# Optimization experiments

Hardware: AMD Instinct MI355X
Metric: run time of the kernel (lower is better)

Reference implementation:

```python
import jax, jax.numpy as jnp
import numpy as np

B, L, C, R = 4, 2048, 64, 8
A_SCALE = 0.1  # keeps spectral radius of per-step A < 1 so 2048-step products stay stable


def setup_inputs() -> dict:
    key = jax.random.key(0)
    k1, k2, k3, k4 = jax.random.split(key, 4)
    A_re = jax.random.normal(k1, (B, L, C, R, R), jnp.float32) * A_SCALE
    A_im = jax.random.normal(k2, (B, L, C, R, R), jnp.float32) * A_SCALE
    X_re = jax.random.normal(k3, (B, L, C, R), jnp.float32)
    X_im = jax.random.normal(k4, (B, L, C, R), jnp.float32)
    return {"A_re": A_re, "A_im": A_im, "X_re": X_re, "X_im": X_im}


def reference(A_re, A_im, X_re, X_im):
    # Complex linear recurrence: Y_t = A_t @ Y_{t-1} + X_t (Y_0 = X_0),
    # computed as a parallel associative scan over the L axis, matching
    # the Triton combine_fn: (a1,x1) o (a2,x2) = (a2@a1, a2@x1 + x2).
    A = jax.lax.complex(A_re, A_im)  # [B,L,C,R,R] complex64
    X = jax.lax.complex(X_re, X_im)  # [B,L,C,R]   complex64

    def combine(left, right):
        a1, x1 = left
        a2, x2 = right
        new_a = jnp.matmul(a2, a1)                          # [.,R,R]@[.,R,R]
        new_x = jnp.einsum('...ij,...j->...i', a2, x1) + x2  # [.,R,R]@[.,R]
        return (new_a, new_x)

    _, Y = jax.lax.associative_scan(combine, (A, X), axis=1)
    # Return real/imag stacked so the output dtype is float32: [B,L,C,R,2]
    return jnp.stack((jnp.real(Y), jnp.imag(Y)), axis=-1)
```

## Files before the change

### kernel.cpp

```cpp
#include <hip/hip_runtime.h>

#define B 4
#define L 2048
#define C 64
#define R 8
#define NCH (B * C)
#define TQ 16
#define S (L / TQ)
#define GRP (NCH / 8)


__global__ __launch_bounds__(64) void k_summary(
    const float* __restrict__ Are, const float* __restrict__ Aim,
    const float* __restrict__ Xre, const float* __restrict__ Xim,
    float2* __restrict__ sumP, float2* __restrict__ sumQ)
{
    __shared__ __align__(16) float sm[1152];
    const int lane = threadIdx.x;
    const int c = lane >> 3, r = lane & 7;
    const int s = blockIdx.x >> 5;
    const int g = blockIdx.x & 31;
    const int n0 = g * 8;
    const int b = n0 >> 6;
    const int cc0 = n0 & (C - 1);
    const int n = n0 + c;
    const int tbase = s * TQ;
    const int sIdx = c * 16 + ((r ^ c) << 1);

    float Pre[8], Pim[8];
#pragma unroll
    for (int k = 0; k < 8; ++k) { Pre[k] = (k == r) ? 1.f : 0.f; Pim[k] = 0.f; }
    float qre = 0.f, qim = 0.f;

    float4 sa0, sa1, si0, si1; float sxr, sxi;
    float4 ta0, ta1, ti0, ti1; float txr, txi;

#define LOADSET1(t, A0, A1, I0, I1, XR, XI)                                    \
    {                                                                          \
        const int fb = (b * L + (t)) * C + cc0;                                \
        const float4* pA = (const float4*)(Are + (long)fb * 64) + lane * 2;    \
        const float4* pI = (const float4*)(Aim + (long)fb * 64) + lane * 2;    \
        A0 = pA[0]; A1 = pA[1]; I0 = pI[0]; I1 = pI[1];                        \
        XR = Xre[(long)fb * 8 + lane]; XI = Xim[(long)fb * 8 + lane];          \
    }

#define STAGESET1(A0, A1, I0, I1, XR, XI)                                      \
    {                                                                          \
        float4* s4 = (float4*)sm;                                              \
        s4[sIdx] = A0; s4[sIdx + 1] = A1;                                      \
        s4[128 + sIdx] = I0; s4[128 + sIdx + 1] = I1;                          \
        sm[1024 + lane] = XR; sm[1088 + lane] = XI;                            \
    }

#define COMPUTE_STEP1()                                                        \
    {                                                                          \
        float xr[8], xi[8];                                                    \
        *(float4*)&xr[0] = *(const float4*)(sm + 1024 + c * 8);                \
        *(float4*)&xr[4] = *(const float4*)(sm + 1024 + c * 8 + 4);            \
        *(float4*)&xi[0] = *(const float4*)(sm + 1088 + c * 8);                \
        *(float4*)&xi[4] = *(const float4*)(sm + 1088 + c * 8 + 4);            \
        _Pragma("unroll")                                                      \
        for (int k = 0; k < 8; ++k) {                                          \
            qre += Pre[k] * xr[k] - Pim[k] * xi[k];                            \
            qim += Pre[k] * xi[k] + Pim[k] * xr[k];                            \
        }                                                                      \
        float Nre[8], Nim[8];                                                  \
        _Pragma("unroll")                                                      \
        for (int j = 0; j < 8; ++j) { Nre[j] = 0.f; Nim[j] = 0.f; }            \
        _Pragma("unroll")                                                      \
        for (int k = 0; k < 8; ++k) {                                          \
            const int ko = ((k ^ c) << 3);    \
            float er[8], ei[8];                                                \
            *(float4*)&er[0] = *(const float4*)(sm + c * 64 + ko);             \
            *(float4*)&er[4] = *(const float4*)(sm + c * 64 + ko + 4);         \
            *(float4*)&ei[0] = *(const float4*)(sm + 512 + c * 64 + ko);       \
            *(float4*)&ei[4] = *(const float4*)(sm + 512 + c * 64 + ko + 4);   \
            const float pr = Pre[k], pi = Pim[k];                              \
            _Pragma("unroll")                                                  \
            for (int j = 0; j < 8; ++j) {                                      \
                Nre[j] += pr * er[j] - pi * ei[j];                             \
                Nim[j] += pr * ei[j] + pi * er[j];                             \
            }                                                                  \
        }                                                                      \
        _Pragma("unroll")                                                      \
        for (int k = 0; k < 8; ++k) { Pre[k] = Nre[k]; Pim[k] = Nim[k]; }      \
    }

    LOADSET1(tbase + TQ - 1, sa0, sa1, si0, si1, sxr, sxi);
    LOADSET1(tbase + TQ - 2, ta0, ta1, ti0, ti1, txr, txi);

#pragma unroll 1
    for (int tt = TQ - 1; tt >= 1; tt -= 2) {
        STAGESET1(sa0, sa1, si0, si1, sxr, sxi);
        if (tt >= 3) LOADSET1(tbase + tt - 2, sa0, sa1, si0, si1, sxr, sxi);
        COMPUTE_STEP1();
        STAGESET1(ta0, ta1, ti0, ti1, txr, txi);
        if (tt >= 3) LOADSET1(tbase + tt - 3, ta0, ta1, ti0, ti1, txr, txi);
        COMPUTE_STEP1();
    }

    float4* gp = (float4*)(sumP + ((long)(s * 256 + n) * 8 + r) * 8);
    gp[0] = make_float4(Pre[0], Pim[0], Pre[1], Pim[1]);
    gp[1] = make_float4(Pre[2], Pim[2], Pre[3], Pim[3]);
    gp[2] = make_float4(Pre[4], Pim[4], Pre[5], Pim[5]);
    gp[3] = make_float4(Pre[6], Pim[6], Pre[7], Pim[7]);
    sumQ[(long)(s * 256 + n) * 8 + r] = make_float2(qre, qim);
}

__global__ __launch_bounds__(64) void k_carry(
    const float2* __restrict__ sumP, const float2* __restrict__ sumQ,
    float2* __restrict__ carry)
{
    __shared__ __align__(16) float cb[160];
    const int lane = threadIdx.x;
    const int c = lane >> 3, r = lane & 7;
    const int n = blockIdx.x * 8 + c;

    float yr = 0.f, yi = 0.f;
    long base = (long)n * 8;
    const float4* prow0 = (const float4*)(sumP + (base + r) * 8);
    float4 p0 = prow0[0], p1 = prow0[1], p2 = prow0[2], p3 = prow0[3];
    float2 qv = sumQ[base + r];

#pragma unroll 1
    for (int s = 0; s < S; ++s) {
        carry[base + r] = make_float2(yr, yi);
        *(float2*)(cb + c * 20 + 2 * r) = make_float2(yr, yi);
        float4 w0 = p0, w1 = p1, w2 = p2, w3 = p3;
        float2 q = qv;
        if (s + 1 < S) {
            const long nb = base + 2048;
            const float4* np = (const float4*)(sumP + (nb + r) * 8);
            p0 = np[0]; p1 = np[1]; p2 = np[2]; p3 = np[3];
            qv = sumQ[nb + r];
        }
        float yvr[8], yvi[8];
        {
            float4 u0 = *(const float4*)(cb + c * 20);
            float4 u1 = *(const float4*)(cb + c * 20 + 4);
            float4 u2 = *(const float4*)(cb + c * 20 + 8);
            float4 u3 = *(const float4*)(cb + c * 20 + 12);
            yvr[0]=u0.x; yvi[0]=u0.y; yvr[1]=u0.z; yvi[1]=u0.w;
            yvr[2]=u1.x; yvi[2]=u1.y; yvr[3]=u1.z; yvi[3]=u1.w;
            yvr[4]=u2.x; yvi[4]=u2.y; yvr[5]=u2.z; yvi[5]=u2.w;
            yvr[6]=u3.x; yvi[6]=u3.y; yvr[7]=u3.z; yvi[7]=u3.w;
        }
        float prr[8], pri[8];
        prr[0]=w0.x; pri[0]=w0.y; prr[1]=w0.z; pri[1]=w0.w;
        prr[2]=w1.x; pri[2]=w1.y; prr[3]=w1.z; pri[3]=w1.w;
        prr[4]=w2.x; pri[4]=w2.y; prr[5]=w2.z; pri[5]=w2.w;
        prr[6]=w3.x; pri[6]=w3.y; prr[7]=w3.z; pri[7]=w3.w;
        float nr0 = q.x, ni0 = q.y, nr1 = 0.f, ni1 = 0.f;
#pragma unroll
        for (int k = 0; k < 8; k += 2) {
            nr0 += prr[k] * yvr[k] - pri[k] * yvi[k];
            ni0 += prr[k] * yvi[k] + pri[k] * yvr[k];
            nr1 += prr[k+1] * yvr[k+1] - pri[k+1] * yvi[k+1];
            ni1 += prr[k+1] * yvi[k+1] + pri[k+1] * yvr[k+1];
        }
        yr = nr0 + nr1; yi = ni0 + ni1;
        base += 2048;
    }
}

__global__ __launch_bounds__(64) void k_fixup(
    const float* __restrict__ Are, const float* __restrict__ Aim,
    const float* __restrict__ Xre, const float* __restrict__ Xim,
    const float2* __restrict__ carry, float2* __restrict__ out)
{
    __shared__ __align__(16) float cb[160];
    const int lane = threadIdx.x;
    const int c = lane >> 3, r = lane & 7;
    const int blk = (int)gridDim.x - 1 - (int)blockIdx.x;
    const int s = blk >> 5;
    const int g = blk & 31;
    const int n0 = g * 8;
    const int b = n0 >> 6;
    const int cc0 = n0 & (C - 1);
    const int n = n0 + c;
    const int tbase = s * TQ;

    float yvr[8], yvi[8];
    {
        const float4* cv = (const float4*)(carry + (long)(s * 256 + n) * 8);
        float4 w0 = cv[0], w1 = cv[1], w2 = cv[2], w3 = cv[3];
        yvr[0]=w0.x; yvi[0]=w0.y; yvr[1]=w0.z; yvi[1]=w0.w;
        yvr[2]=w1.x; yvi[2]=w1.y; yvr[3]=w1.z; yvi[3]=w1.w;
        yvr[4]=w2.x; yvi[4]=w2.y; yvr[5]=w2.z; yvi[5]=w2.w;
        yvr[6]=w3.x; yvi[6]=w3.y; yvr[7]=w3.z; yvi[7]=w3.w;
    }

    float4 sa0, sa1, si0, si1; float sxr, sxi;
    float4 ta0, ta1, ti0, ti1; float txr, txi;

#define LOADSET3(t, A0, A1, I0, I1, XR, XI)                                    \
    {                                                                          \
        const int fb = (b * L + (t)) * C + cc0;                                \
        const float4* pA = (const float4*)(Are + (long)fb * 64) + lane * 2;    \
        const float4* pI = (const float4*)(Aim + (long)fb * 64) + lane * 2;    \
        A0 = pA[0]; A1 = pA[1]; I0 = pI[0]; I1 = pI[1];                        \
        XR = Xre[(long)fb * 8 + lane]; XI = Xim[(long)fb * 8 + lane];          \
    }

#define FIX_STEP(A0, A1, I0, I1, XR_, XI_, t)                                  \
    {                                                                          \
        float nr0 = (XR_), ni0 = (XI_), nr1 = 0.f, ni1 = 0.f;                  \
        nr0 += A0.x * yvr[0] - I0.x * yvi[0];                                  \
        ni0 += A0.x * yvi[0] + I0.x * yvr[0];                                  \
        nr1 += A0.y * yvr[1] - I0.y * yvi[1];                                  \
        ni1 += A0.y * yvi[1] + I0.y * yvr[1];                                  \
        nr0 += A0.z * yvr[2] - I0.z * yvi[2];                                  \
        ni0 += A0.z * yvi[2] + I0.z * yvr[2];                                  \
        nr1 += A0.w * yvr[3] - I0.w * yvi[3];                                  \
        ni1 += A0.w * yvi[3] + I0.w * yvr[3];                                  \
        nr0 += A1.x * yvr[4] - I1.x * yvi[4];                                  \
        ni0 += A1.x * yvi[4] + I1.x * yvr[4];                                  \
        nr1 += A1.y * yvr[5] - I1.y * yvi[5];                                  \
        ni1 += A1.y * yvi[5] + I1.y * yvr[5];                                  \
        nr0 += A1.z * yvr[6] - I1.z * yvi[6];                                  \
        ni0 += A1.z * yvi[6] + I1.z * yvr[6];                                  \
        nr1 += A1.w * yvr[7] - I1.w * yvi[7];                                  \
        ni1 += A1.w * yvi[7] + I1.w * yvr[7];                                  \
        const float nr = nr0 + nr1, ni = ni0 + ni1;                            \
        const int fb = (b * L + (t)) * C + cc0;                                \
        out[(long)fb * 8 + lane] = make_float2(nr, ni);                        \
        *(float2*)(cb + c * 20 + 2 * r) = make_float2(nr, ni);                 \
        float4 u0 = *(const float4*)(cb + c * 20);                             \
        float4 u1 = *(const float4*)(cb + c * 20 + 4);                         \
        float4 u2 = *(const float4*)(cb + c * 20 + 8);                         \
        float4 u3 = *(const float4*)(cb + c * 20 + 12);                        \
        yvr[0]=u0.x; yvi[0]=u0.y; yvr[1]=u0.z; yvi[1]=u0.w;                    \
        yvr[2]=u1.x; yvi[2]=u1.y; yvr[3]=u1.z; yvi[3]=u1.w;                    \
        yvr[4]=u2.x; yvi[4]=u2.y; yvr[5]=u2.z; yvi[5]=u2.w;                    \
        yvr[6]=u3.x; yvi[6]=u3.y; yvr[7]=u3.z; yvi[7]=u3.w;                    \
    }

    LOADSET3(tbase + 0, sa0, sa1, si0, si1, sxr, sxi);
    LOADSET3(tbase + 1, ta0, ta1, ti0, ti1, txr, txi);

#pragma unroll 1
    for (int tt = 0; tt < TQ; tt += 2) {
        float4 A0 = sa0, A1 = sa1, I0 = si0, I1 = si1;
        float XR = sxr, XI = sxi;
        if (tt + 2 < TQ) LOADSET3(tbase + tt + 2, sa0, sa1, si0, si1, sxr, sxi);
        FIX_STEP(A0, A1, I0, I1, XR, XI, tbase + tt);
        float4 B0 = ta0, B1 = ta1, J0 = ti0, J1 = ti1;
        float YR = txr, YI = txi;
        if (tt + 3 < TQ) LOADSET3(tbase + tt + 3, ta0, ta1, ti0, ti1, txr, txi);
        FIX_STEP(B0, B1, J0, J1, YR, YI, tbase + tt + 1);
    }
}

extern "C" void kernel_launch(void* const* d_in, const int* in_sizes, int n_in,
                              void* d_out, int out_size, void* d_ws, size_t ws_size,
                              hipStream_t stream)
{
    const float* Are = (const float*)d_in[0];
    const float* Aim = (const float*)d_in[1];
    const float* Xre = (const float*)d_in[2];
    const float* Xim = (const float*)d_in[3];
    float2* out = (float2*)d_out;

    float2* sumP  = (float2*)d_ws;
    float2* sumQ  = sumP + (long)S * NCH * 64;
    float2* carry = sumQ + (long)S * NCH * 8;

    k_summary<<<S * GRP, 64, 0, stream>>>(Are, Aim, Xre, Xim, sumP, sumQ);
    k_carry<<<NCH / 8, 64, 0, stream>>>(sumP, sumQ, carry);
    k_fixup<<<S * GRP, 64, 0, stream>>>(Are, Aim, Xre, Xim, carry, out);
}
```

Measured before the change: 432.5 us.

## Use async global-to-LDS loads, 4-wave blocks, and shuffles for vector broadcast

The summary kernel now streams A and X tiles straight into double-buffered LDS with global_load_lds and explicit vmcnt waits, replacing the register staging and LDS store round trip. Both the summary and fixup kernels pack four independent wavefronts per 256-thread block. The carry and fixup kernels broadcast the state vector with cross-lane shuffles instead of an LDS write/read. This is meant to cut load latency and LDS traffic, but it relies on hand-written waitcnt accounting and needs more LDS per block.

```diff
diff --git a/kernel.cpp b/kernel.cpp
--- a/kernel.cpp
+++ b/kernel.cpp
@@ -10,55 +10,62 @@
 #define GRP (NCH / 8)
 
 
-__global__ __launch_bounds__(64) void k_summary(
+#define GLL(gp, lp, sz)                                                        \
+    __builtin_amdgcn_global_load_lds(                                          \
+        (const __attribute__((address_space(1))) void*)(gp),                   \
+        (__attribute__((address_space(3))) void*)(lp), sz, 0, 0)
+
+__global__ __launch_bounds__(256) void k_summary(
     const float* __restrict__ Are, const float* __restrict__ Aim,
     const float* __restrict__ Xre, const float* __restrict__ Xim,
     float2* __restrict__ sumP, float2* __restrict__ sumQ)
 {
-    __shared__ __align__(16) float sm[1152];
-    const int lane = threadIdx.x;
+    __shared__ __align__(16) float sm[4 * 2 * 1152];
+    const int lane = threadIdx.x & 63;
+    const int w = __builtin_amdgcn_readfirstlane((int)(threadIdx.x >> 6));
     const int c = lane >> 3, r = lane & 7;
-    const int s = blockIdx.x >> 5;
-    const int g = blockIdx.x & 31;
+    const int s = blockIdx.x >> 3;
+    const int g = (blockIdx.x & 7) * 4 + w;
     const int n0 = g * 8;
     const int b = n0 >> 6;
     const int cc0 = n0 & (C - 1);
     const int n = n0 + c;
     const int tbase = s * TQ;
-    const int sIdx = c * 16 + ((r ^ c) << 1);
+
+    const int q = (lane >> 1) & 7, h = lane & 1;
+    const int c0 = lane >> 4, c1 = 4 + (lane >> 4);
+    const int o0 = c0 * 16 + ((q ^ c0) << 1) + h;
+    const int o1 = c1 * 16 + ((q ^ c1) << 1) + h;
+
+    char* lw = ((char*)sm) + w * 9216;
+    const float* wb = sm + w * 2304;
 
     float Pre[8], Pim[8];
 #pragma unroll
     for (int k = 0; k < 8; ++k) { Pre[k] = (k == r) ? 1.f : 0.f; Pim[k] = 0.f; }
     float qre = 0.f, qim = 0.f;
 
-    float4 sa0, sa1, si0, si1; float sxr, sxi;
-    float4 ta0, ta1, ti0, ti1; float txr, txi;
-
-#define LOADSET1(t, A0, A1, I0, I1, XR, XI)                                    \
+#define ISSUE1(t, bf)                                                          \
     {                                                                          \
         const int fb = (b * L + (t)) * C + cc0;                                \
-        const float4* pA = (const float4*)(Are + (long)fb * 64) + lane * 2;    \
-        const float4* pI = (const float4*)(Aim + (long)fb * 64) + lane * 2;    \
-        A0 = pA[0]; A1 = pA[1]; I0 = pI[0]; I1 = pI[1];                        \
-        XR = Xre[(long)fb * 8 + lane]; XI = Xim[(long)fb * 8 + lane];          \
-    }
-
-#define STAGESET1(A0, A1, I0, I1, XR, XI)                                      \
-    {                                                                          \
-        float4* s4 = (float4*)sm;                                              \
-        s4[sIdx] = A0; s4[sIdx + 1] = A1;                                      \
-        s4[128 + sIdx] = I0; s4[128 + sIdx + 1] = I1;                          \
-        sm[1024 + lane] = XR; sm[1088 + lane] = XI;                            \
-    }
-
-#define COMPUTE_STEP1()                                                        \
+        const float4* gA = (const float4*)(Are + (long)fb * 64);               \
+        const float4* gI = (const float4*)(Aim + (long)fb * 64);               \
+        char* lb = lw + (bf) * 4608;                                           \
+        GLL(gA + o0, lb, 16);                                                  \
+        GLL(gA + o1, lb + 1024, 16);                                           \
+        GLL(gI + o0, lb + 2048, 16);                                           \
+        GLL(gI + o1, lb + 3072, 16);                                           \
+        GLL(Xre + (long)fb * 8 + lane, lb + 4096, 4);                          \
+        GLL(Xim + (long)fb * 8 + lane, lb + 4352, 4);                          \
+    }
+
+#define COMPUTE_STEP1(bp)                                                      \
     {                                                                          \
         float xr[8], xi[8];                                                    \
-        *(float4*)&xr[0] = *(const float4*)(sm + 1024 + c * 8);                \
-        *(float4*)&xr[4] = *(const float4*)(sm + 1024 + c * 8 + 4);            \
-        *(float4*)&xi[0] = *(const float4*)(sm + 1088 + c * 8);                \
-        *(float4*)&xi[4] = *(const float4*)(sm + 1088 + c * 8 + 4);            \
+        *(float4*)&xr[0] = *(const float4*)((bp) + 1024 + c * 8);              \
+        *(float4*)&xr[4] = *(const float4*)((bp) + 1024 + c * 8 + 4);          \
+        *(float4*)&xi[0] = *(const float4*)((bp) + 1088 + c * 8);              \
+        *(float4*)&xi[4] = *(const float4*)((bp) + 1088 + c * 8 + 4);          \
         _Pragma("unroll")                                                      \
         for (int k = 0; k < 8; ++k) {                                          \
             qre += Pre[k] * xr[k] - Pim[k] * xi[k];                            \
@@ -69,12 +76,12 @@
         for (int j = 0; j < 8; ++j) { Nre[j] = 0.f; Nim[j] = 0.f; }            \
         _Pragma("unroll")                                                      \
         for (int k = 0; k < 8; ++k) {                                          \
-            const int ko = ((k ^ c) << 3);    \
+            const int ko = ((k ^ c) << 3);                                     \
             float er[8], ei[8];                                                \
-            *(float4*)&er[0] = *(const float4*)(sm + c * 64 + ko);             \
-            *(float4*)&er[4] = *(const float4*)(sm + c * 64 + ko + 4);         \
-            *(float4*)&ei[0] = *(const float4*)(sm + 512 + c * 64 + ko);       \
-            *(float4*)&ei[4] = *(const float4*)(sm + 512 + c * 64 + ko + 4);   \
+            *(float4*)&er[0] = *(const float4*)((bp) + c * 64 + ko);           \
+            *(float4*)&er[4] = *(const float4*)((bp) + c * 64 + ko + 4);       \
+            *(float4*)&ei[0] = *(const float4*)((bp) + 512 + c * 64 + ko);     \
+            *(float4*)&ei[4] = *(const float4*)((bp) + 512 + c * 64 + ko + 4); \
             const float pr = Pre[k], pi = Pim[k];                              \
             _Pragma("unroll")                                                  \
             for (int j = 0; j < 8; ++j) {                                      \
@@ -86,17 +93,20 @@
         for (int k = 0; k < 8; ++k) { Pre[k] = Nre[k]; Pim[k] = Nim[k]; }      \
     }
 
-    LOADSET1(tbase + TQ - 1, sa0, sa1, si0, si1, sxr, sxi);
-    LOADSET1(tbase + TQ - 2, ta0, ta1, ti0, ti1, txr, txi);
-
+    ISSUE1(tbase + TQ - 1, 0);
 #pragma unroll 1
-    for (int tt = TQ - 1; tt >= 1; tt -= 2) {
-        STAGESET1(sa0, sa1, si0, si1, sxr, sxi);
-        if (tt >= 3) LOADSET1(tbase + tt - 2, sa0, sa1, si0, si1, sxr, sxi);
-        COMPUTE_STEP1();
-        STAGESET1(ta0, ta1, ti0, ti1, txr, txi);
-        if (tt >= 3) LOADSET1(tbase + tt - 3, ta0, ta1, ti0, ti1, txr, txi);
-        COMPUTE_STEP1();
+    for (int tt = 0; tt < TQ - 1; ++tt) {
+        ISSUE1(tbase + TQ - 2 - tt, (tt + 1) & 1);
+        asm volatile("s_waitcnt vmcnt(6)" ::: "memory");
+        __builtin_amdgcn_sched_barrier(0);
+        const float* bp = wb + (tt & 1) * 1152;
+        COMPUTE_STEP1(bp);
+    }
+    asm volatile("s_waitcnt vmcnt(0)" ::: "memory");
+    __builtin_amdgcn_sched_barrier(0);
+    {
+        const float* bp = wb + ((TQ - 1) & 1) * 1152;
+        COMPUTE_STEP1(bp);
     }
 
     float4* gp = (float4*)(sumP + ((long)(s * 256 + n) * 8 + r) * 8);
@@ -111,7 +121,6 @@
     const float2* __restrict__ sumP, const float2* __restrict__ sumQ,
     float2* __restrict__ carry)
 {
-    __shared__ __align__(16) float cb[160];
     const int lane = threadIdx.x;
     const int c = lane >> 3, r = lane & 7;
     const int n = blockIdx.x * 8 + c;
@@ -125,32 +134,26 @@
 #pragma unroll 1
     for (int s = 0; s < S; ++s) {
         carry[base + r] = make_float2(yr, yi);
-        *(float2*)(cb + c * 20 + 2 * r) = make_float2(yr, yi);
+        float yvr[8], yvi[8];
+#pragma unroll
+        for (int k = 0; k < 8; ++k) {
+            yvr[k] = __shfl(yr, (c << 3) + k, 64);
+            yvi[k] = __shfl(yi, (c << 3) + k, 64);
+        }
         float4 w0 = p0, w1 = p1, w2 = p2, w3 = p3;
-        float2 q = qv;
+        float2 qq = qv;
         if (s + 1 < S) {
             const long nb = base + 2048;
             const float4* np = (const float4*)(sumP + (nb + r) * 8);
             p0 = np[0]; p1 = np[1]; p2 = np[2]; p3 = np[3];
             qv = sumQ[nb + r];
         }
-        float yvr[8], yvi[8];
-        {
-            float4 u0 = *(const float4*)(cb + c * 20);
-            float4 u1 = *(const float4*)(cb + c * 20 + 4);
-            float4 u2 = *(const float4*)(cb + c * 20 + 8);
-            float4 u3 = *(const float4*)(cb + c * 20 + 12);
-            yvr[0]=u0.x; yvi[0]=u0.y; yvr[1]=u0.z; yvi[1]=u0.w;
-            yvr[2]=u1.x; yvi[2]=u1.y; yvr[3]=u1.z; yvi[3]=u1.w;
-            yvr[4]=u2.x; yvi[4]=u2.y; yvr[5]=u2.z; yvi[5]=u2.w;
-            yvr[6]=u3.x; yvi[6]=u3.y; yvr[7]=u3.z; yvi[7]=u3.w;
-        }
         float prr[8], pri[8];
         prr[0]=w0.x; pri[0]=w0.y; prr[1]=w0.z; pri[1]=w0.w;
         prr[2]=w1.x; pri[2]=w1.y; prr[3]=w1.z; pri[3]=w1.w;
         prr[4]=w2.x; pri[4]=w2.y; prr[5]=w2.z; pri[5]=w2.w;
         prr[6]=w3.x; pri[6]=w3.y; prr[7]=w3.z; pri[7]=w3.w;
-        float nr0 = q.x, ni0 = q.y, nr1 = 0.f, ni1 = 0.f;
+        float nr0 = qq.x, ni0 = qq.y, nr1 = 0.f, ni1 = 0.f;
 #pragma unroll
         for (int k = 0; k < 8; k += 2) {
             nr0 += prr[k] * yvr[k] - pri[k] * yvi[k];
@@ -163,17 +166,17 @@
     }
 }
 
-__global__ __launch_bounds__(64) void k_fixup(
+__global__ __launch_bounds__(256) void k_fixup(
     const float* __restrict__ Are, const float* __restrict__ Aim,
     const float* __restrict__ Xre, const float* __restrict__ Xim,
     const float2* __restrict__ carry, float2* __restrict__ out)
 {
-    __shared__ __align__(16) float cb[160];
-    const int lane = threadIdx.x;
+    const int lane = threadIdx.x & 63;
+    const int w = threadIdx.x >> 6;
     const int c = lane >> 3, r = lane & 7;
     const int blk = (int)gridDim.x - 1 - (int)blockIdx.x;
-    const int s = blk >> 5;
-    const int g = blk & 31;
+    const int s = blk >> 3;
+    const int g = (blk & 7) * 4 + w;
     const int n0 = g * 8;
     const int b = n0 >> 6;
     const int cc0 = n0 & (C - 1);
@@ -224,15 +227,11 @@
         const float nr = nr0 + nr1, ni = ni0 + ni1;                            \
         const int fb = (b * L + (t)) * C + cc0;                                \
         out[(long)fb * 8 + lane] = make_float2(nr, ni);                        \
-        *(float2*)(cb + c * 20 + 2 * r) = make_float2(nr, ni);                 \
-        float4 u0 = *(const float4*)(cb + c * 20);                             \
-        float4 u1 = *(const float4*)(cb + c * 20 + 4);                         \
-        float4 u2 = *(const float4*)(cb + c * 20 + 8);                         \
-        float4 u3 = *(const float4*)(cb + c * 20 + 12);                        \
-        yvr[0]=u0.x; yvi[0]=u0.y; yvr[1]=u0.z; yvi[1]=u0.w;                    \
-        yvr[2]=u1.x; yvi[2]=u1.y; yvr[3]=u1.z; yvi[3]=u1.w;                    \
-        yvr[4]=u2.x; yvi[4]=u2.y; yvr[5]=u2.z; yvi[5]=u2.w;                    \
-        yvr[6]=u3.x; yvi[6]=u3.y; yvr[7]=u3.z; yvi[7]=u3.w;                    \
+        _Pragma("unroll")                                                      \
+        for (int k = 0; k < 8; ++k) {                                          \
+            yvr[k] = __shfl(nr, (c << 3) + k, 64);                             \
+            yvi[k] = __shfl(ni, (c << 3) + k, 64);                             \
+        }                                                                      \
     }
 
     LOADSET3(tbase + 0, sa0, sa1, si0, si1, sxr, sxi);
@@ -265,7 +264,7 @@
     float2* sumQ  = sumP + (long)S * NCH * 64;
     float2* carry = sumQ + (long)S * NCH * 8;
 
-    k_summary<<<S * GRP, 64, 0, stream>>>(Are, Aim, Xre, Xim, sumP, sumQ);
+    k_summary<<<(S * GRP) / 4, 256, 0, stream>>>(Are, Aim, Xre, Xim, sumP, sumQ);
     k_carry<<<NCH / 8, 64, 0, stream>>>(sumP, sumQ, carry);
-    k_fixup<<<S * GRP, 64, 0, stream>>>(Are, Aim, Xre, Xim, carry, out);
-}
+    k_fixup<<<(S * GRP) / 4, 256, 0, stream>>>(Are, Aim, Xre, Xim, carry, out);
+}
```

After: 456.2 us. +5.5%, slower.
